# Kernel optimization log

Measured on AMD Instinct MI355X. Metric: run time of the kernel, lower is better.

Reference implementation:

```python
import jax, jax.numpy as jnp
import numpy as np

EMBED_DIM = 1024
NUM_HEADS = 16
HEAD_DIM = EMBED_DIM // NUM_HEADS
ALPHA = 0.5  # mirror_bias['alpha'] default


def setup_inputs() -> dict:
    key = jax.random.key(0)
    k_x, k_m, kq, kk, kv, ko = jax.random.split(key, 6)
    B, S = 2, 2048
    x = jax.random.normal(k_x, (B, S, EMBED_DIM), dtype=jnp.float32)
    mask = jax.random.bernoulli(k_m, 0.1, (B, S))  # True = masked-out key (padding)
    # xavier_uniform for square [E,E]: limit = sqrt(6/(E+E))
    lim = float(np.sqrt(6.0 / (EMBED_DIM + EMBED_DIM)))
    Wq = jax.random.uniform(kq, (EMBED_DIM, EMBED_DIM), jnp.float32, -lim, lim)
    Wk = jax.random.uniform(kk, (EMBED_DIM, EMBED_DIM), jnp.float32, -lim, lim)
    Wv = jax.random.uniform(kv, (EMBED_DIM, EMBED_DIM), jnp.float32, -lim, lim)
    Wo = jax.random.uniform(ko, (EMBED_DIM, EMBED_DIM), jnp.float32, -lim, lim)
    return {"x": x, "Wq": Wq, "Wk": Wk, "Wv": Wv, "Wo": Wo, "mask": mask}


def _heads(t, B, S):
    # [B,S,E] -> [B,H,S,D]
    return t.reshape(B, S, NUM_HEADS, HEAD_DIM).transpose(0, 2, 1, 3)


def reference(x, Wq, Wk, Wv, Wo, mask):
    B, S, E = x.shape
    # nn.Linear(bias=False): y = x @ W.T
    q = _heads(x @ Wq.T, B, S)
    k = _heads(x @ Wk.T, B, S)
    v = _heads(x @ Wv.T, B, S)
    scores = jnp.einsum('bhqd,bhkd->bhqk', q, k) / jnp.sqrt(jnp.float32(HEAD_DIM))
    # mirror positional bias: target j = S-1-i
    i_idx = jnp.arange(S)[:, None]
    j_idx = jnp.arange(S)[None, :]
    dist = jnp.abs(j_idx - (S - 1 - i_idx)).astype(jnp.float32)
    bias = -ALPHA * (dist / jnp.float32(S))  # [S_q, S_k]
    scores = scores + bias[None, None, :, :]
    # bool 2D mask -> key padding mask [B,1,1,S_k], True = -inf
    scores = jnp.where(mask[:, None, None, :], -jnp.inf, scores)
    attn = jax.nn.softmax(scores, axis=-1)
    out = jnp.einsum('bhqk,bhkd->bhqd', attn, v)
    out = out.transpose(0, 2, 1, 3).reshape(B, S, E)
    return out @ Wo.T
```

## Files before the change

### kernel.cpp

```cpp
#include <hip/hip_runtime.h>

typedef unsigned short u16;
typedef unsigned int u32;
typedef unsigned long long u64;
typedef __attribute__((ext_vector_type(8))) short bf16x8;
typedef __attribute__((ext_vector_type(4))) float f32x4;
typedef __attribute__((ext_vector_type(2))) unsigned int u32x2;

#define MFMA16(A, B, C) __builtin_amdgcn_mfma_f32_16x16x32_bf16(A, B, C, 0, 0, 0)

__device__ __forceinline__ u16 f2bf(float f) {
  union { float f; unsigned u; } x; x.f = f;
  unsigned r = x.u + 0x7fffu + ((x.u >> 16) & 1u);
  return (u16)(r >> 16);
}

__device__ __forceinline__ u32 pack_bf2(float a, float b) {
  u32 r;
  asm("v_cvt_pk_bf16_f32 %0, %1, %2" : "=v"(r) : "v"(a), "v"(b));
  return r;
}

__device__ __forceinline__ void gload_lds16(const u16* g, u16* l) {
  __builtin_amdgcn_global_load_lds((const __attribute__((address_space(1))) void*)g,
                                   (__attribute__((address_space(3))) void*)l,
                                   16, 0, 0);
}

__global__ __launch_bounds__(256) void cvt_all(const float* __restrict__ x,
                                               const float* __restrict__ Wq,
                                               const float* __restrict__ Wk,
                                               const float* __restrict__ Wv,
                                               const float* __restrict__ Wo,
                                               const int* __restrict__ mask,
                                               u16* __restrict__ xb,
                                               u16* __restrict__ Wqkvb,
                                               u16* __restrict__ Wob,
                                               u32* __restrict__ mbits,
                                               int NE, int NW, int NB) {
  if ((int)blockIdx.x == NB) {
    const int t = threadIdx.x;
    if (t < 128) {
      const int* m = mask + t * 32;
      u32 w = 0;
#pragma unroll
      for (int j = 0; j < 32; j++) w |= (m[j] != 0 ? 1u : 0u) << j;
      mbits[t] = w;
    }
    return;
  }
  const int e = (blockIdx.x * 256 + threadIdx.x) * 8;
  const float* s;
  u16* d;
  if (e < NE) { s = x + e; d = xb + e; }
  else {
    int f = e - NE;
    if (f < 3 * NW) {
      d = Wqkvb + f;
      s = (f < NW) ? Wq + f : (f < 2 * NW) ? Wk + (f - NW) : Wv + (f - 2 * NW);
    } else { f -= 3 * NW; s = Wo + f; d = Wob + f; }
  }
  const float4 a = *(const float4*)s;
  const float4 b = *(const float4*)(s + 4);
  bf16x8 o;
  o[0] = (short)f2bf(a.x); o[1] = (short)f2bf(a.y);
  o[2] = (short)f2bf(a.z); o[3] = (short)f2bf(a.w);
  o[4] = (short)f2bf(b.x); o[5] = (short)f2bf(b.y);
  o[6] = (short)f2bf(b.z); o[7] = (short)f2bf(b.w);
  *(bf16x8*)d = o;
}

__global__ __launch_bounds__(256) void gemm_qkv(const u16* __restrict__ A,
                                                const u16* __restrict__ B,
                                                u16* __restrict__ Qo,
                                                u16* __restrict__ Ko,
                                                u16* __restrict__ Vto,
                                                int M, int N, int K) {
  __shared__ alignas(16) u16 As[128 * 64];
  __shared__ alignas(16) u16 Bs[128 * 64];
  const int t = threadIdx.x;
  const int lane = t & 63, wave = t >> 6;
  const int quad = lane >> 4, l16 = lane & 15;
  const int m0 = blockIdx.y * 128, n0 = blockIdx.x * 128;
  const int wm = (wave >> 1) * 64, wn = (wave & 1) * 64;
  const int sx = l16 & 7;

  f32x4 acc[4][4] = {};

  for (int kk = 0; kk < K; kk += 64) {
#pragma unroll
    for (int i = 0; i < 4; i++) {
      const int c = t + i * 256;
      const int row = c >> 3, sub = c & 7;
      const int col = ((sub ^ (row & 7)) * 8);
      gload_lds16(A + (size_t)(m0 + row) * K + kk + col, As + (size_t)c * 8);
      gload_lds16(B + (size_t)(n0 + row) * K + kk + col, Bs + (size_t)c * 8);
    }
    __syncthreads();

#pragma unroll
    for (int ks = 0; ks < 2; ks++) {
      bf16x8 af[4], bfr[4];
#pragma unroll
      for (int i = 0; i < 4; i++)
        af[i] = *(const bf16x8*)(As + (wm + i * 16 + l16) * 64 +
                                 ((ks * 4 + quad) ^ sx) * 8);
#pragma unroll
      for (int j = 0; j < 4; j++)
        bfr[j] = *(const bf16x8*)(Bs + (wn + j * 16 + l16) * 64 +
                                  ((ks * 4 + quad) ^ sx) * 8);
#pragma unroll
      for (int i = 0; i < 4; i++)
#pragma unroll
        for (int j = 0; j < 4; j++)
          acc[i][j] = MFMA16(af[i], bfr[j], acc[i][j]);
    }
    __syncthreads();
  }

  const int G = ((m0 + wm) & 2047) >> 6;
#pragma unroll
  for (int j = 0; j < 4; j++) {
    const int col = n0 + wn + j * 16 + l16;
    if (col < 1024) {
#pragma unroll
      for (int i = 0; i < 4; i++)
#pragma unroll
        for (int r = 0; r < 4; r++)
          Qo[(size_t)(m0 + wm + i * 16 + quad * 4 + r) * 1024 + col] =
              f2bf(acc[i][j][r]);
    } else if (col < 2048) {
#pragma unroll
      for (int i = 0; i < 4; i++)
#pragma unroll
        for (int r = 0; r < 4; r++)
          Ko[(size_t)(m0 + wm + i * 16 + quad * 4 + r) * 1024 + (col - 1024)] =
              f2bf(acc[i][j][r]);
    } else {
      u16* base = Vto + ((size_t)(m0 >> 11) * 1024 + (col - 2048)) * 2048 + G * 64;
#pragma unroll
      for (int r = 0; r < 4; r++) {
        u32x2 v;
        v.x = pack_bf2(acc[0][j][r], acc[1][j][r]);
        v.y = pack_bf2(acc[2][j][r], acc[3][j][r]);
        *(u32x2*)(base + 4 * (quad * 4 + r)) = v;
      }
    }
  }
}

__global__ __launch_bounds__(256) void gemm_out(const u16* __restrict__ A,
                                                const u16* __restrict__ B,
                                                float* __restrict__ C,
                                                int M, int N, int K) {
  __shared__ alignas(16) u16 As[128 * 64];
  __shared__ alignas(16) u16 Bs[64 * 64];
  const int t = threadIdx.x;
  const int lane = t & 63, wave = t >> 6;
  const int quad = lane >> 4, l16 = lane & 15;
  const int m0 = blockIdx.y * 128, n0 = blockIdx.x * 64;
  const int wm = (wave >> 1) * 64, wn = (wave & 1) * 32;
  const int sx = l16 & 7;

  f32x4 acc[4][2] = {};

  for (int kk = 0; kk < K; kk += 64) {
#pragma unroll
    for (int i = 0; i < 4; i++) {
      const int c = t + i * 256;
      const int row = c >> 3, sub = c & 7;
      gload_lds16(A + (size_t)(m0 + row) * K + kk + ((sub ^ (row & 7)) * 8),
                  As + (size_t)c * 8);
    }
#pragma unroll
    for (int i = 0; i < 2; i++) {
      const int c = t + i * 256;
      const int row = c >> 3, sub = c & 7;
      gload_lds16(B + (size_t)(n0 + row) * K + kk + ((sub ^ (row & 7)) * 8),
                  Bs + (size_t)c * 8);
    }
    __syncthreads();

#pragma unroll
    for (int ks = 0; ks < 2; ks++) {
      bf16x8 af[4], bfr[2];
#pragma unroll
      for (int i = 0; i < 4; i++)
        af[i] = *(const bf16x8*)(As + (wm + i * 16 + l16) * 64 +
                                 ((ks * 4 + quad) ^ sx) * 8);
#pragma unroll
      for (int j = 0; j < 2; j++)
        bfr[j] = *(const bf16x8*)(Bs + (wn + j * 16 + l16) * 64 +
                                  ((ks * 4 + quad) ^ sx) * 8);
#pragma unroll
      for (int i = 0; i < 4; i++)
#pragma unroll
        for (int j = 0; j < 2; j++)
          acc[i][j] = MFMA16(af[i], bfr[j], acc[i][j]);
    }
    __syncthreads();
  }

#pragma unroll
  for (int i = 0; i < 4; i++)
#pragma unroll
    for (int j = 0; j < 2; j++)
#pragma unroll
      for (int r = 0; r < 4; r++)
        C[(size_t)(m0 + wm + i * 16 + quad * 4 + r) * N + n0 + wn + j * 16 + l16] =
            acc[i][j][r];
}

__global__ __launch_bounds__(256) void attn_fwd(const u16* __restrict__ Q,
                                                const u16* __restrict__ Kb_,
                                                const u16* __restrict__ Vt,
                                                const u32* __restrict__ mbits,
                                                float* __restrict__ OP0,
                                                float* __restrict__ OP1,
                                                float* __restrict__ Lp) {
  constexpr int S = 2048, E = 1024;
  __shared__ alignas(16) u16 Ks[2][64 * 64];
  __shared__ alignas(16) u16 Vs[2][64 * 64];
  __shared__ alignas(16) u32 Pl[4][16 * 32];
  const int t = threadIdx.x;
  const int lane = t & 63, wave = t >> 6;
  const int quad = lane >> 4, l16 = lane & 15;
  const int bh = blockIdx.y, b = bh >> 4, h = bh & 15;
  const int sp = blockIdx.z;
  const int kbase0 = sp * 1024;
  const int q0 = blockIdx.x * 128 + wave * 32;

  const int c0 = t, c1 = t + 256;
  const int kr0 = c0 >> 3, kr1 = c1 >> 3;
  const int kcol0 = ((c0 & 7) ^ (kr0 & 7)) * 8;
  const int kcol1 = ((c1 & 7) ^ (kr1 & 7)) * 8;
  const u16* kP0 = Kb_ + (size_t)(b * S + kbase0 + kr0) * E + h * 64 + kcol0;
  const u16* kP1 = Kb_ + (size_t)(b * S + kbase0 + kr1) * E + h * 64 + kcol1;
  const u16* vbase = Vt + (size_t)(b * 16 + h) * 64 * S + kbase0;
  const u16* vP0 = vbase + (size_t)kr0 * S + kcol0;
  const u16* vP1 = vbase + (size_t)kr1 * S + kcol1;

  bf16x8 aq[2][2];
#pragma unroll
  for (int qt = 0; qt < 2; qt++) {
    const u16* qp = Q + ((size_t)(b * S) + q0 + qt * 16 + l16) * E + h * 64;
    aq[qt][0] = *(const bf16x8*)(qp + quad * 8);
    aq[qt][1] = *(const bf16x8*)(qp + 32 + quad * 8);
  }

  const u32* mb = mbits + b * 64;
  const int sx = l16 & 7;
  const int pkey = l16 & 14;

  float lr[2][4] = {};
  f32x4 accO[2][4] = {};
  const float fq0 = (float)(q0 + quad * 4 - 2047);

  const float K1 = 0.125f * 1.44269504f;
  const float K2 = 2.44140625e-4f * 1.44269504f;
  const float K3 = -8.0f * 1.44269504f;
  const float KM = -1e6f;

  gload_lds16(kP0, Ks[0] + c0 * 8);
  gload_lds16(kP1, Ks[0] + c1 * 8);
  gload_lds16(vP0, Vs[0] + c0 * 8);
  gload_lds16(vP1, Vs[0] + c1 * 8);
  __syncthreads();

  int buf = 0;
  for (int kc = 0; kc < 1024; kc += 64) {
    if (kc + 64 < 1024) {
      const int kn = kc + 64;
      gload_lds16(kP0 + (size_t)kn * E, Ks[buf ^ 1] + c0 * 8);
      gload_lds16(kP1 + (size_t)kn * E, Ks[buf ^ 1] + c1 * 8);
      gload_lds16(vP0 + kn, Vs[buf ^ 1] + c0 * 8);
      gload_lds16(vP1 + kn, Vs[buf ^ 1] + c1 * 8);
    }
    const u16* ks = Ks[buf];
    const u16* vs = Vs[buf];
    u32* pl = Pl[wave];

    bf16x8 bk[4][2];
#pragma unroll
    for (int T = 0; T < 4; T++)
#pragma unroll
      for (int dh = 0; dh < 2; dh++)
        bk[T][dh] = *(const bf16x8*)(ks + (T * 16 + l16) * 64 +
                                     ((dh * 4 + quad) ^ sx) * 8);

    f32x4 s[2][4] = {};
#pragma unroll
    for (int qt = 0; qt < 2; qt++)
#pragma unroll
      for (int T = 0; T < 4; T++) {
        s[qt][T] = MFMA16(aq[qt][0], bk[T][0], s[qt][T]);
        s[qt][T] = MFMA16(aq[qt][1], bk[T][1], s[qt][T]);
      }

    const int kabs = kbase0 + kc;
    const u64 mw = *(const u64*)(mb + (kabs >> 5));
    const u32 mlo = (u32)mw, mhi = (u32)(mw >> 32);
    const float B0 = ((mlo >> l16) & 1) ? KM : K3;
    const float B1 = ((mlo >> (l16 + 16)) & 1) ? KM : K3;
    const float B2 = ((mhi >> l16) & 1) ? KM : K3;
    const float B3 = ((mhi >> (l16 + 16)) & 1) ? KM : K3;
    const float kl = (float)(kabs + l16);

    u32x2 pk1[4];
#pragma unroll
    for (int qt = 0; qt < 2; qt++)
#pragma unroll
      for (int r = 0; r < 4; r++) {
        const float fb = kl + fq0 + (float)(qt * 16 + r);
        const float p0 = __builtin_amdgcn_exp2f(
            fmaf(fabsf(fb), -K2, fmaf(s[qt][0][r], K1, B0)));
        const float p1 = __builtin_amdgcn_exp2f(
            fmaf(fabsf(fb + 16.f), -K2, fmaf(s[qt][1][r], K1, B1)));
        const float p2 = __builtin_amdgcn_exp2f(
            fmaf(fabsf(fb + 32.f), -K2, fmaf(s[qt][2][r], K1, B2)));
        const float p3 = __builtin_amdgcn_exp2f(
            fmaf(fabsf(fb + 48.f), -K2, fmaf(s[qt][3][r], K1, B3)));
        lr[qt][r] += (p0 + p1) + (p2 + p3);
        u32x2 v;
        v.x = pack_bf2(p0, p1);
        v.y = pack_bf2(p2, p3);
        if (qt == 0) {
          const int m = quad * 4 + r;
          *(u32x2*)(pl + m * 32 + 2 * (l16 ^ (m & 14))) = v;
        } else {
          pk1[r] = v;
        }
      }

    bf16x8 bv[2][4];
#pragma unroll
    for (int kst = 0; kst < 2; kst++)
#pragma unroll
      for (int tt = 0; tt < 4; tt++)
        bv[kst][tt] = *(const bf16x8*)(vs + (tt * 16 + l16) * 64 +
                                       ((kst * 4 + quad) ^ sx) * 8);

    asm volatile("s_waitcnt lgkmcnt(0)" ::: "memory");
    bf16x8 ap0[2];
#pragma unroll
    for (int kst = 0; kst < 2; kst++)
      ap0[kst] = *(const bf16x8*)(pl + l16 * 32 + 2 * ((kst * 8 + 2 * quad) ^ pkey));
#pragma unroll
    for (int kst = 0; kst < 2; kst++)
#pragma unroll
      for (int tt = 0; tt < 4; tt++)
        accO[0][tt] = MFMA16(ap0[kst], bv[kst][tt], accO[0][tt]);

    asm volatile("" ::: "memory");
#pragma unroll
    for (int r = 0; r < 4; r++) {
      const int m = quad * 4 + r;
      *(u32x2*)(pl + m * 32 + 2 * (l16 ^ (m & 14))) = pk1[r];
    }
    asm volatile("s_waitcnt lgkmcnt(0)" ::: "memory");
    bf16x8 ap1[2];
#pragma unroll
    for (int kst = 0; kst < 2; kst++)
      ap1[kst] = *(const bf16x8*)(pl + l16 * 32 + 2 * ((kst * 8 + 2 * quad) ^ pkey));
#pragma unroll
    for (int kst = 0; kst < 2; kst++)
#pragma unroll
      for (int tt = 0; tt < 4; tt++)
        accO[1][tt] = MFMA16(ap1[kst], bv[kst][tt], accO[1][tt]);

    __syncthreads();
    buf ^= 1;
  }

  float* OP = sp ? OP1 : OP0;
#pragma unroll
  for (int qt = 0; qt < 2; qt++)
#pragma unroll
    for (int r = 0; r < 4; r++) {
      float l = lr[qt][r];
      l += __shfl_xor(l, 1);
      l += __shfl_xor(l, 2);
      l += __shfl_xor(l, 4);
      l += __shfl_xor(l, 8);
      const int qg = q0 + qt * 16 + quad * 4 + r;
      const size_t row = ((size_t)bh << 11) + qg;
      float* orow = OP + row * 64;
#pragma unroll
      for (int tt = 0; tt < 4; tt++) orow[tt * 16 + l16] = accO[qt][tt][r];
      if (l16 == 0) Lp[((size_t)sp << 16) + row] = l;
    }
}

__global__ __launch_bounds__(256) void attn_merge(const float* __restrict__ OP0,
                                                  const float* __restrict__ OP1,
                                                  const float* __restrict__ Lp,
                                                  u16* __restrict__ Ao) {
  const int i = blockIdx.x * 256 + threadIdx.x;
  const int row = i >> 4;
  const int d4 = (i & 15) * 4;
  const float inv = 1.0f / (Lp[row] + Lp[65536 + row]);
  const float4 a = *(const float4*)(OP0 + (size_t)row * 64 + d4);
  const float4 c = *(const float4*)(OP1 + (size_t)row * 64 + d4);
  const int bb = row >> 15, h = (row >> 11) & 15, q = row & 2047;
  u32x2 v;
  v.x = pack_bf2((a.x + c.x) * inv, (a.y + c.y) * inv);
  v.y = pack_bf2((a.z + c.z) * inv, (a.w + c.w) * inv);
  *(u32x2*)(Ao + (size_t)((bb << 11) + q) * 1024 + h * 64 + d4) = v;
}

extern "C" void kernel_launch(void* const* d_in, const int* in_sizes, int n_in,
                              void* d_out, int out_size, void* d_ws, size_t ws_size,
                              hipStream_t stream) {
  const float* x  = (const float*)d_in[0];
  const float* Wq = (const float*)d_in[1];
  const float* Wk = (const float*)d_in[2];
  const float* Wv = (const float*)d_in[3];
  const float* Wo = (const float*)d_in[4];
  const int* mask = (const int*)d_in[5];

  const int M = 4096, N = 1024, K = 1024;
  const int NE = M * N, NW = N * K;
  const int NB = (NE + 4 * NW) / 2048;

  u16* xb    = (u16*)d_ws;
  u16* Wqkvb = xb + NE;
  u16* Wob   = Wqkvb + (size_t)3 * NW;
  u16* Qb    = Wob + NW;
  u16* Kb    = Qb + NE;
  u16* Vt    = Kb + NE;
  u16* Ao    = Vt + NE;
  u32* mbits = (u32*)(Ao + NE);
  float* OP1 = (float*)(mbits + 128);
  float* Lp  = OP1 + (size_t)65536 * 64;
  float* OP0 = (float*)d_out;

  cvt_all<<<NB + 1, 256, 0, stream>>>(x, Wq, Wk, Wv, Wo, mask,
                                      xb, Wqkvb, Wob, mbits, NE, NW, NB);

  gemm_qkv<<<dim3(3072 / 128, M / 128), 256, 0, stream>>>(
      xb, Wqkvb, Qb, Kb, Vt, M, 3072, K);
  attn_fwd<<<dim3(16, 32, 2), 256, 0, stream>>>(Qb, Kb, Vt, mbits,
                                                OP0, OP1, Lp);
  attn_merge<<<4096, 256, 0, stream>>>(OP0, OP1, Lp, Ao);
  gemm_out<<<dim3(N / 64, M / 128), 256, 0, stream>>>(
      Ao, Wob, (float*)d_out, M, N, K);
}
```

Before: 204.8 us.

## Compute transposed scores to keep P in registers, drop LDS round-trip

The QK^T MFMA operands are swapped so the scores come out transposed, letting the softmax probabilities be packed straight into MFMA A-operand registers. This removes the per-wave LDS staging of P and its waitcnt barriers. The key-mask bitmask is replaced with a precomputed float bias array (mask plus constant offset) read as vectors. The V-transpose stores in the QKV GEMM are widened to 16-byte writes, and s_setprio hints are placed around the MFMA phases. Row sums now need only cross-quad shuffles, at the cost of extra global loads of the mask bias per tile and a changed V layout that must match the attention reads.

```diff
diff --git a/kernel.cpp b/kernel.cpp
--- a/kernel.cpp
+++ b/kernel.cpp
@@ -6,6 +6,7 @@
 typedef __attribute__((ext_vector_type(8))) short bf16x8;
 typedef __attribute__((ext_vector_type(4))) float f32x4;
 typedef __attribute__((ext_vector_type(2))) unsigned int u32x2;
+typedef __attribute__((ext_vector_type(4))) unsigned int u32x4;
 
 #define MFMA16(A, B, C) __builtin_amdgcn_mfma_f32_16x16x32_bf16(A, B, C, 0, 0, 0)
 
@@ -36,16 +37,22 @@
                                                u16* __restrict__ xb,
                                                u16* __restrict__ Wqkvb,
                                                u16* __restrict__ Wob,
-                                               u32* __restrict__ mbits,
+                                               float* __restrict__ Mbg,
                                                int NE, int NW, int NB) {
   if ((int)blockIdx.x == NB) {
     const int t = threadIdx.x;
-    if (t < 128) {
-      const int* m = mask + t * 32;
-      u32 w = 0;
-#pragma unroll
-      for (int j = 0; j < 32; j++) w |= (m[j] != 0 ? 1u : 0u) << j;
-      mbits[t] = w;
+    const int j0 = t * 16;
+    const float K3C = -8.0f * 1.44269504f;
+    const float KMS = K3C - 1.0e6f;
+#pragma unroll
+    for (int jj = 0; jj < 16; jj += 4) {
+      const int4 m4 = *(const int4*)(mask + j0 + jj);
+      float4 o;
+      o.x = m4.x ? KMS : K3C;
+      o.y = m4.y ? KMS : K3C;
+      o.z = m4.z ? KMS : K3C;
+      o.w = m4.w ? KMS : K3C;
+      *(float4*)(Mbg + j0 + jj) = o;
     }
     return;
   }
@@ -138,13 +145,18 @@
               f2bf(acc[i][j][r]);
     } else {
       u16* base = Vto + ((size_t)(m0 >> 11) * 1024 + (col - 2048)) * 2048 + G * 64;
-#pragma unroll
-      for (int r = 0; r < 4; r++) {
-        u32x2 v;
-        v.x = pack_bf2(acc[0][j][r], acc[1][j][r]);
-        v.y = pack_bf2(acc[2][j][r], acc[3][j][r]);
-        *(u32x2*)(base + 4 * (quad * 4 + r)) = v;
-      }
+      const int C = 8 * (quad & 1) + 16 * (quad >> 1);
+      u32x4 w0, w1;
+      w0.x = pack_bf2(acc[0][j][0], acc[0][j][1]);
+      w0.y = pack_bf2(acc[0][j][2], acc[0][j][3]);
+      w0.z = pack_bf2(acc[1][j][0], acc[1][j][1]);
+      w0.w = pack_bf2(acc[1][j][2], acc[1][j][3]);
+      w1.x = pack_bf2(acc[2][j][0], acc[2][j][1]);
+      w1.y = pack_bf2(acc[2][j][2], acc[2][j][3]);
+      w1.z = pack_bf2(acc[3][j][0], acc[3][j][1]);
+      w1.w = pack_bf2(acc[3][j][2], acc[3][j][3]);
+      *(u32x4*)(base + C) = w0;
+      *(u32x4*)(base + C + 32) = w1;
     }
   }
 }
@@ -214,14 +226,13 @@
 __global__ __launch_bounds__(256) void attn_fwd(const u16* __restrict__ Q,
                                                 const u16* __restrict__ Kb_,
                                                 const u16* __restrict__ Vt,
-                                                const u32* __restrict__ mbits,
+                                                const float* __restrict__ Mb,
                                                 float* __restrict__ OP0,
                                                 float* __restrict__ OP1,
                                                 float* __restrict__ Lp) {
   constexpr int S = 2048, E = 1024;
   __shared__ alignas(16) u16 Ks[2][64 * 64];
   __shared__ alignas(16) u16 Vs[2][64 * 64];
-  __shared__ alignas(16) u32 Pl[4][16 * 32];
   const int t = threadIdx.x;
   const int lane = t & 63, wave = t >> 6;
   const int quad = lane >> 4, l16 = lane & 15;
@@ -248,18 +259,15 @@
     aq[qt][1] = *(const bf16x8*)(qp + 32 + quad * 8);
   }
 
-  const u32* mb = mbits + b * 64;
+  const float* mbp = Mb + b * 2048 + kbase0 + quad * 4;
   const int sx = l16 & 7;
-  const int pkey = l16 & 14;
-
-  float lr[2][4] = {};
+
+  float lr[2] = {};
   f32x4 accO[2][4] = {};
-  const float fq0 = (float)(q0 + quad * 4 - 2047);
+  const float fb0 = (float)(kbase0 + quad * 4 + q0 + l16 - 2047);
 
   const float K1 = 0.125f * 1.44269504f;
   const float K2 = 2.44140625e-4f * 1.44269504f;
-  const float K3 = -8.0f * 1.44269504f;
-  const float KM = -1e6f;
 
   gload_lds16(kP0, Ks[0] + c0 * 8);
   gload_lds16(kP1, Ks[0] + c1 * 8);
@@ -276,9 +284,12 @@
       gload_lds16(vP0 + kn, Vs[buf ^ 1] + c0 * 8);
       gload_lds16(vP1 + kn, Vs[buf ^ 1] + c1 * 8);
     }
+    f32x4 mv[4];
+#pragma unroll
+    for (int T = 0; T < 4; T++) mv[T] = *(const f32x4*)(mbp + kc + 16 * T);
+
     const u16* ks = Ks[buf];
     const u16* vs = Vs[buf];
-    u32* pl = Pl[wave];
 
     bf16x8 bk[4][2];
 #pragma unroll
@@ -289,84 +300,54 @@
                                      ((dh * 4 + quad) ^ sx) * 8);
 
     f32x4 s[2][4] = {};
+    __builtin_amdgcn_s_setprio(1);
 #pragma unroll
     for (int qt = 0; qt < 2; qt++)
 #pragma unroll
       for (int T = 0; T < 4; T++) {
-        s[qt][T] = MFMA16(aq[qt][0], bk[T][0], s[qt][T]);
-        s[qt][T] = MFMA16(aq[qt][1], bk[T][1], s[qt][T]);
+        s[qt][T] = MFMA16(bk[T][0], aq[qt][0], s[qt][T]);
+        s[qt][T] = MFMA16(bk[T][1], aq[qt][1], s[qt][T]);
       }
-
-    const int kabs = kbase0 + kc;
-    const u64 mw = *(const u64*)(mb + (kabs >> 5));
-    const u32 mlo = (u32)mw, mhi = (u32)(mw >> 32);
-    const float B0 = ((mlo >> l16) & 1) ? KM : K3;
-    const float B1 = ((mlo >> (l16 + 16)) & 1) ? KM : K3;
-    const float B2 = ((mhi >> l16) & 1) ? KM : K3;
-    const float B3 = ((mhi >> (l16 + 16)) & 1) ? KM : K3;
-    const float kl = (float)(kabs + l16);
-
-    u32x2 pk1[4];
+    __builtin_amdgcn_s_setprio(0);
+
+    const float fbL = fb0 + (float)kc;
+
+    u32 pw[2][2][4];
 #pragma unroll
     for (int qt = 0; qt < 2; qt++)
 #pragma unroll
-      for (int r = 0; r < 4; r++) {
-        const float fb = kl + fq0 + (float)(qt * 16 + r);
-        const float p0 = __builtin_amdgcn_exp2f(
-            fmaf(fabsf(fb), -K2, fmaf(s[qt][0][r], K1, B0)));
-        const float p1 = __builtin_amdgcn_exp2f(
-            fmaf(fabsf(fb + 16.f), -K2, fmaf(s[qt][1][r], K1, B1)));
-        const float p2 = __builtin_amdgcn_exp2f(
-            fmaf(fabsf(fb + 32.f), -K2, fmaf(s[qt][2][r], K1, B2)));
-        const float p3 = __builtin_amdgcn_exp2f(
-            fmaf(fabsf(fb + 48.f), -K2, fmaf(s[qt][3][r], K1, B3)));
-        lr[qt][r] += (p0 + p1) + (p2 + p3);
-        u32x2 v;
-        v.x = pack_bf2(p0, p1);
-        v.y = pack_bf2(p2, p3);
-        if (qt == 0) {
-          const int m = quad * 4 + r;
-          *(u32x2*)(pl + m * 32 + 2 * (l16 ^ (m & 14))) = v;
-        } else {
-          pk1[r] = v;
+      for (int T = 0; T < 4; T++) {
+        float p[4];
+#pragma unroll
+        for (int r = 0; r < 4; r++) {
+          const float fe = fbL + (float)(16 * T + 16 * qt + r);
+          const float tv = fmaf(s[qt][T][r], K1, mv[T][r]);
+          p[r] = __builtin_amdgcn_exp2f(fmaf(fabsf(fe), -K2, tv));
         }
+        lr[qt] += (p[0] + p[1]) + (p[2] + p[3]);
+        pw[qt][T >> 1][(T & 1) * 2 + 0] = pack_bf2(p[0], p[1]);
+        pw[qt][T >> 1][(T & 1) * 2 + 1] = pack_bf2(p[2], p[3]);
       }
 
-    bf16x8 bv[2][4];
-#pragma unroll
-    for (int kst = 0; kst < 2; kst++)
+    __builtin_amdgcn_s_setprio(1);
+#pragma unroll
+    for (int kst = 0; kst < 2; kst++) {
+      bf16x8 bv[4];
 #pragma unroll
       for (int tt = 0; tt < 4; tt++)
-        bv[kst][tt] = *(const bf16x8*)(vs + (tt * 16 + l16) * 64 +
-                                       ((kst * 4 + quad) ^ sx) * 8);
-
-    asm volatile("s_waitcnt lgkmcnt(0)" ::: "memory");
-    bf16x8 ap0[2];
-#pragma unroll
-    for (int kst = 0; kst < 2; kst++)
-      ap0[kst] = *(const bf16x8*)(pl + l16 * 32 + 2 * ((kst * 8 + 2 * quad) ^ pkey));
-#pragma unroll
-    for (int kst = 0; kst < 2; kst++)
-#pragma unroll
-      for (int tt = 0; tt < 4; tt++)
-        accO[0][tt] = MFMA16(ap0[kst], bv[kst][tt], accO[0][tt]);
-
-    asm volatile("" ::: "memory");
-#pragma unroll
-    for (int r = 0; r < 4; r++) {
-      const int m = quad * 4 + r;
-      *(u32x2*)(pl + m * 32 + 2 * (l16 ^ (m & 14))) = pk1[r];
-    }
-    asm volatile("s_waitcnt lgkmcnt(0)" ::: "memory");
-    bf16x8 ap1[2];
-#pragma unroll
-    for (int kst = 0; kst < 2; kst++)
-      ap1[kst] = *(const bf16x8*)(pl + l16 * 32 + 2 * ((kst * 8 + 2 * quad) ^ pkey));
-#pragma unroll
-    for (int kst = 0; kst < 2; kst++)
-#pragma unroll
-      for (int tt = 0; tt < 4; tt++)
-        accO[1][tt] = MFMA16(ap1[kst], bv[kst][tt], accO[1][tt]);
+        bv[tt] = *(const bf16x8*)(vs + (tt * 16 + l16) * 64 +
+                                  ((kst * 4 + quad) ^ sx) * 8);
+#pragma unroll
+      for (int qt = 0; qt < 2; qt++) {
+        union { u32 w[4]; bf16x8 v; } ap;
+        ap.w[0] = pw[qt][kst][0]; ap.w[1] = pw[qt][kst][1];
+        ap.w[2] = pw[qt][kst][2]; ap.w[3] = pw[qt][kst][3];
+#pragma unroll
+        for (int tt = 0; tt < 4; tt++)
+          accO[qt][tt] = MFMA16(ap.v, bv[tt], accO[qt][tt]);
+      }
+    }
+    __builtin_amdgcn_s_setprio(0);
 
     __syncthreads();
     buf ^= 1;
@@ -374,20 +355,22 @@
 
   float* OP = sp ? OP1 : OP0;
 #pragma unroll
+  for (int qt = 0; qt < 2; qt++) {
+    float l = lr[qt];
+    l += __shfl_xor(l, 16);
+    l += __shfl_xor(l, 32);
+    if (lane < 16)
+      Lp[((size_t)sp << 16) + ((size_t)bh << 11) + q0 + qt * 16 + l16] = l;
+  }
+#pragma unroll
   for (int qt = 0; qt < 2; qt++)
 #pragma unroll
     for (int r = 0; r < 4; r++) {
-      float l = lr[qt][r];
-      l += __shfl_xor(l, 1);
-      l += __shfl_xor(l, 2);
-      l += __shfl_xor(l, 4);
-      l += __shfl_xor(l, 8);
       const int qg = q0 + qt * 16 + quad * 4 + r;
       const size_t row = ((size_t)bh << 11) + qg;
       float* orow = OP + row * 64;
 #pragma unroll
       for (int tt = 0; tt < 4; tt++) orow[tt * 16 + l16] = accO[qt][tt][r];
-      if (l16 == 0) Lp[((size_t)sp << 16) + row] = l;
     }
 }
 
@@ -429,17 +412,17 @@
   u16* Kb    = Qb + NE;
   u16* Vt    = Kb + NE;
   u16* Ao    = Vt + NE;
-  u32* mbits = (u32*)(Ao + NE);
-  float* OP1 = (float*)(mbits + 128);
+  float* Mbg = (float*)(Ao + NE);
+  float* OP1 = Mbg + 4096;
   float* Lp  = OP1 + (size_t)65536 * 64;
   float* OP0 = (float*)d_out;
 
   cvt_all<<<NB + 1, 256, 0, stream>>>(x, Wq, Wk, Wv, Wo, mask,
-                                      xb, Wqkvb, Wob, mbits, NE, NW, NB);
+                                      xb, Wqkvb, Wob, Mbg, NE, NW, NB);
 
   gemm_qkv<<<dim3(3072 / 128, M / 128), 256, 0, stream>>>(
       xb, Wqkvb, Qb, Kb, Vt, M, 3072, K);
-  attn_fwd<<<dim3(16, 32, 2), 256, 0, stream>>>(Qb, Kb, Vt, mbits,
+  attn_fwd<<<dim3(16, 32, 2), 256, 0, stream>>>(Qb, Kb, Vt, Mbg,
                                                 OP0, OP1, Lp);
   attn_merge<<<4096, 256, 0, stream>>>(OP0, OP1, Lp, Ao);
   gemm_out<<<dim3(N / 64, M / 128), 256, 0, stream>>>(
```

Measured after the change: 202.1 us. No clear change (-1.3%).
